# Kernel tuning notes

Hardware: AMD Instinct MI355X
Metric: run time of the kernel (lower is better)

Reference implementation:

```python
import jax, jax.numpy as jnp
import numpy as np

B, S, H, F, E, TOP_K = 2, 2048, 1024, 2048, 8, 2


def setup_inputs() -> dict:
    key = jax.random.key(0)
    ks = jax.random.split(key, 5)
    scale_h = 1.0 / np.sqrt(H)
    scale_f = 1.0 / np.sqrt(F)
    return {
        "hidden_states": jax.random.normal(ks[0], (B, S, H), jnp.float32),
        "gate_w": jax.random.normal(ks[1], (H, E), jnp.float32) * scale_h,
        "w_up": jax.random.normal(ks[2], (E, H, F), jnp.float32) * scale_h,
        "w_gate": jax.random.normal(ks[3], (E, H, F), jnp.float32) * scale_h,
        "w_down": jax.random.normal(ks[4], (E, F, H), jnp.float32) * scale_f,
    }


def reference(hidden_states, gate_w, w_up, w_gate, w_down):
    b, s, h = hidden_states.shape
    x = hidden_states.reshape(-1, h)                      # [T, H]
    T = x.shape[0]

    # Router: softmax then top-k then renormalize (as in the module)
    router_logits = x @ gate_w                            # [T, E]
    probs = jax.nn.softmax(router_logits, axis=-1)
    routing_weights, selected_experts = jax.lax.top_k(probs, TOP_K)  # [T, K]
    routing_weights = routing_weights / jnp.sum(routing_weights, axis=-1, keepdims=True)
    routing_weights = routing_weights.astype(x.dtype)

    # Per-token combine weight for each expert (sum over k where selected == e).
    # Equals the masked where/+ accumulation in the original (zero where unselected).
    combine = jnp.zeros((T, E), x.dtype).at[
        jnp.arange(T)[:, None], selected_experts
    ].add(routing_weights)                                # [T, E]

    # Dense expert compute on ALL tokens for every expert (faithful to original,
    # where each device runs its expert on the full token set, then psum).
    up = jnp.einsum("th,ehf->etf", x, w_up)               # [E, T, F]
    gate = jnp.einsum("th,ehf->etf", x, w_gate)           # [E, T, F]
    inner = jax.nn.silu(up) * gate                        # note: silu on up_proj, as in source
    expert_out = jnp.einsum("etf,efh->eth", inner, w_down)  # [E, T, H]

    # Weighted combine == psum over expert axis of masked/weighted outputs.
    y = jnp.einsum("te,eth->th", combine, expert_out)     # [T, H]
    return y.reshape(b, s, h)
```

## Files before the change

### kernel.cpp

```cpp
#include <hip/hip_runtime.h>
#include <hip/hip_bf16.h>

typedef __bf16 bf16x8 __attribute__((ext_vector_type(8)));
typedef float f32x4 __attribute__((ext_vector_type(4)));

#define T_TOK 4096
#define H_DIM 1024
#define F_DIM 2048
#define NEXP 8
#define TOTROWS 8192
#define MAXTILES 80

__device__ inline unsigned short f2b(float f) {
    unsigned int u = __float_as_uint(f);
    unsigned int r = (u + 0x7fffu + ((u >> 16) & 1u)) >> 16;
    return (unsigned short)r;
}

__device__ inline void gload16(const void* g, void* l) {
    __builtin_amdgcn_global_load_lds(
        (const __attribute__((address_space(1))) unsigned int*)g,
        (__attribute__((address_space(3))) unsigned int*)l,
        16, 0, 0);
}

__global__ __launch_bounds__(256) void router_kernel(const float* __restrict__ x,
                                                     const float* __restrict__ gw,
                                                     int* __restrict__ sel, float* __restrict__ selw) {
    int t = blockIdx.x * 4 + (threadIdx.x >> 6);
    int lane = threadIdx.x & 63;
    float acc[8] = {0.f,0.f,0.f,0.f,0.f,0.f,0.f,0.f};
    const float* xr = x + (size_t)t * H_DIM;
    for (int h = lane; h < H_DIM; h += 64) {
        float xv = xr[h];
        const float4* g = (const float4*)(gw + h * 8);
        float4 g0 = g[0], g1 = g[1];
        acc[0] += xv * g0.x; acc[1] += xv * g0.y; acc[2] += xv * g0.z; acc[3] += xv * g0.w;
        acc[4] += xv * g1.x; acc[5] += xv * g1.y; acc[6] += xv * g1.z; acc[7] += xv * g1.w;
    }
#pragma unroll
    for (int off = 32; off >= 1; off >>= 1)
#pragma unroll
        for (int e = 0; e < 8; ++e)
            acc[e] += __shfl_down(acc[e], off);
    if (lane == 0) {
        float mx = acc[0];
#pragma unroll
        for (int e = 1; e < 8; ++e) mx = fmaxf(mx, acc[e]);
        float p[8]; float s = 0.f;
#pragma unroll
        for (int e = 0; e < 8; ++e) { p[e] = expf(acc[e] - mx); s += p[e]; }
        float inv_s = 1.f / s;
#pragma unroll
        for (int e = 0; e < 8; ++e) p[e] *= inv_s;
        int e1 = 0; float p1 = p[0];
#pragma unroll
        for (int e = 1; e < 8; ++e) if (p[e] > p1) { p1 = p[e]; e1 = e; }
        int e2 = -1; float p2 = -1.f;
#pragma unroll
        for (int e = 0; e < 8; ++e) { if (e == e1) continue; if (p[e] > p2) { p2 = p[e]; e2 = e; } }
        float inv = 1.f / (p1 + p2);
        sel[t * 2 + 0] = e1; sel[t * 2 + 1] = e2;
        selw[t * 2 + 0] = p1 * inv; selw[t * 2 + 1] = p2 * inv;
    }
}

__global__ __launch_bounds__(256) void scan_kernel(const int* __restrict__ sel,
                                                   int* __restrict__ cnt, int* __restrict__ off,
                                                   int* __restrict__ fill,
                                                   int* __restrict__ tileExp, int* __restrict__ tileM0) {
    __shared__ int h[NEXP];
    int tid = threadIdx.x;
    if (tid < NEXP) h[tid] = 0;
    __syncthreads();
    for (int i = tid; i < TOTROWS; i += 256) atomicAdd(&h[sel[i]], 1);
    __syncthreads();
    if (tid == 0) {
        int o = 0;
        for (int e = 0; e < NEXP; ++e) { cnt[e] = h[e]; off[e] = o; o += h[e]; fill[e] = 0; }
        int nt = 0;
        for (int e = 0; e < NEXP; ++e)
            for (int m0 = 0; m0 < h[e]; m0 += 128) { tileExp[nt] = e; tileM0[nt] = m0; nt++; }
        for (int i = nt; i < MAXTILES; ++i) { tileExp[i] = -1; tileM0[i] = 0; }
    }
}

__global__ __launch_bounds__(256) void scatgath_kernel(const int* __restrict__ sel,
                                                       const float* __restrict__ selw,
                                                       const int* __restrict__ off,
                                                       int* __restrict__ fill,
                                                       float* __restrict__ rowWgt,
                                                       int* __restrict__ tokRow,
                                                       const float* __restrict__ x,
                                                       unsigned short* __restrict__ Xg) {
    __shared__ int rs[2];
    int t = blockIdx.x;
    int tid = threadIdx.x;
    if (tid == 0) {
#pragma unroll
        for (int k = 0; k < 2; ++k) {
            int e = sel[t * 2 + k];
            int slot = atomicAdd(&fill[e], 1);
            int r = off[e] + slot;
            rowWgt[r] = selw[t * 2 + k];
            tokRow[t * 2 + k] = r;
            rs[k] = r;
        }
    }
    __syncthreads();
    int r1 = rs[0], r2 = rs[1];
    float4 v = ((const float4*)(x + (size_t)t * H_DIM))[tid];
    ushort4 o;
    o.x = f2b(v.x); o.y = f2b(v.y); o.z = f2b(v.z); o.w = f2b(v.w);
    ((ushort4*)(Xg + (size_t)r1 * H_DIM))[tid] = o;
    ((ushort4*)(Xg + (size_t)r2 * H_DIM))[tid] = o;
}

__global__ __launch_bounds__(256) void transpose_cvt_kernel(
        const float* __restrict__ w_up, const float* __restrict__ w_gate,
        const float* __restrict__ w_down,
        unsigned short* __restrict__ wTu, unsigned short* __restrict__ wTg,
        unsigned short* __restrict__ wTd) {
    __shared__ unsigned short lt[64 * 68];
    int z = blockIdx.z;
    int e = blockIdx.y;
    const float* src; unsigned short* dst; int R, C, tr, tc;
    if (z == 0)      { src = w_up;   dst = wTu; R = H_DIM; C = F_DIM; }
    else if (z == 1) { src = w_gate; dst = wTg; R = H_DIM; C = F_DIM; }
    else             { src = w_down; dst = wTd; R = F_DIM; C = H_DIM; }
    if (R == H_DIM) { tc = blockIdx.x & 31; tr = blockIdx.x >> 5; }
    else            { tc = blockIdx.x & 15; tr = blockIdx.x >> 4; }
    const float* s = src + (size_t)e * H_DIM * F_DIM;
    unsigned short* d = dst + (size_t)e * H_DIM * F_DIM;
    int r0 = tr * 64, c0 = tc * 64;
    int tid = threadIdx.x;
    int fc = tid & 15, row = tid >> 4;
#pragma unroll
    for (int i = 0; i < 4; ++i) {
        int r = row + i * 16;
        float4 v = *(const float4*)(s + (size_t)(r0 + r) * C + c0 + fc * 4);
        lt[(fc * 4 + 0) * 68 + r] = f2b(v.x);
        lt[(fc * 4 + 1) * 68 + r] = f2b(v.y);
        lt[(fc * 4 + 2) * 68 + r] = f2b(v.z);
        lt[(fc * 4 + 3) * 68 + r] = f2b(v.w);
    }
    __syncthreads();
    int ch = tid & 7, cc = tid >> 3;
#pragma unroll
    for (int i = 0; i < 2; ++i) {
        int c = cc + i * 32;
        uint2 lo = *(const uint2*)&lt[c * 68 + ch * 8];
        uint2 hi = *(const uint2*)&lt[c * 68 + ch * 8 + 4];
        uint4 o = make_uint4(lo.x, lo.y, hi.x, hi.y);
        *(uint4*)(d + (size_t)(c0 + c) * R + r0 + ch * 8) = o;
    }
}

__global__ __launch_bounds__(256, 2) void gemm_upgate_kernel(
        const unsigned short* __restrict__ Xg,
        const unsigned short* __restrict__ wTu,
        const unsigned short* __restrict__ wTg,
        unsigned short* __restrict__ inner,
        const int* __restrict__ tileExp, const int* __restrict__ tileM0,
        const int* __restrict__ off, const int* __restrict__ cnt) {
    __shared__ __align__(16) unsigned short la[128 * 64];
    __shared__ __align__(16) unsigned short lbu[128 * 64];
    __shared__ __align__(16) unsigned short lbg[128 * 64];
    int bt = blockIdx.y;
    int e = tileExp[bt];
    if (e < 0) return;
    int m0 = tileM0[bt];
    int r0 = off[e] + m0;
    int valid = cnt[e] - m0;
    int f0 = blockIdx.x * 128;
    const unsigned short* aB = Xg + (size_t)r0 * H_DIM;
    const unsigned short* bu = wTu + (size_t)e * F_DIM * H_DIM + (size_t)f0 * H_DIM;
    const unsigned short* bg = wTg + (size_t)e * F_DIM * H_DIM + (size_t)f0 * H_DIM;
    int tid = threadIdx.x;
    int lane = tid & 63, wid = tid >> 6;
    int wm = wid >> 1, wn = wid & 1;
    int l16 = lane & 15, quad = lane >> 4;

    int srcOff[4];
#pragma unroll
    for (int it = 0; it < 4; ++it) {
        int chunk = it * 256 + tid;
        int row = chunk >> 3;
        srcOff[it] = row * H_DIM + (((chunk & 7) ^ (row & 7)) << 3);
    }
    f32x4 accU[4][4], accG[4][4];
#pragma unroll
    for (int i = 0; i < 4; ++i)
#pragma unroll
        for (int j = 0; j < 4; ++j) { accU[i][j] = (f32x4)0.f; accG[i][j] = (f32x4)0.f; }

    for (int k0 = 0; k0 < H_DIM; k0 += 64) {
        __syncthreads();
#pragma unroll
        for (int it = 0; it < 4; ++it) {
            int lbase = it * 2048 + wid * 512;
            gload16(aB + srcOff[it] + k0, &la[lbase]);
            gload16(bu + srcOff[it] + k0, &lbu[lbase]);
            gload16(bg + srcOff[it] + k0, &lbg[lbase]);
        }
        __syncthreads();
#pragma unroll
        for (int h = 0; h < 2; ++h) {
            bf16x8 af[4], bfu[4], bfg[4];
#pragma unroll
            for (int i = 0; i < 4; ++i) {
                int lr = wm * 64 + i * 16 + l16;
                af[i] = *(const bf16x8*)&la[lr * 64 + ((((h * 4 + quad) ^ (lr & 7))) << 3)];
            }
#pragma unroll
            for (int j = 0; j < 4; ++j) {
                int lr = wn * 64 + j * 16 + l16;
                int p = lr * 64 + ((((h * 4 + quad) ^ (lr & 7))) << 3);
                bfu[j] = *(const bf16x8*)&lbu[p];
                bfg[j] = *(const bf16x8*)&lbg[p];
            }
#pragma unroll
            for (int i = 0; i < 4; ++i)
#pragma unroll
                for (int j = 0; j < 4; ++j) {
                    accU[i][j] = __builtin_amdgcn_mfma_f32_16x16x32_bf16(af[i], bfu[j], accU[i][j], 0, 0, 0);
                    accG[i][j] = __builtin_amdgcn_mfma_f32_16x16x32_bf16(af[i], bfg[j], accG[i][j], 0, 0, 0);
                }
        }
    }
#pragma unroll
    for (int i = 0; i < 4; ++i) {
#pragma unroll
        for (int rr = 0; rr < 4; ++rr) {
            int ml = wm * 64 + i * 16 + quad * 4 + rr;
            if (ml >= valid) continue;
            size_t base = (size_t)(r0 + ml) * F_DIM + f0;
#pragma unroll
            for (int j = 0; j < 4; ++j) {
                float u = accU[i][j][rr];
                float g = accG[i][j][rr];
                float v = u / (1.f + expf(-u)) * g;
                inner[base + wn * 64 + j * 16 + l16] = f2b(v);
            }
        }
    }
}

__global__ __launch_bounds__(256, 2) void gemm_down_kernel(
        const unsigned short* __restrict__ inner,
        const unsigned short* __restrict__ wTd,
        float* __restrict__ part,
        const int* __restrict__ tileExp, const int* __restrict__ tileM0,
        const int* __restrict__ off, const int* __restrict__ cnt,
        const float* __restrict__ rowWgt) {
    __shared__ __align__(16) unsigned short la[128 * 64];
    __shared__ __align__(16) unsigned short lb[128 * 64];
    int bt = blockIdx.y;
    int e = tileExp[bt];
    if (e < 0) return;
    int m0 = tileM0[bt];
    int r0 = off[e] + m0;
    int valid = cnt[e] - m0;
    int h0 = blockIdx.x * 128;
    const unsigned short* aB = inner + (size_t)r0 * F_DIM;
    const unsigned short* bp = wTd + (size_t)e * H_DIM * F_DIM + (size_t)h0 * F_DIM;
    int tid = threadIdx.x;
    int lane = tid & 63, wid = tid >> 6;
    int wm = wid >> 1, wn = wid & 1;
    int l16 = lane & 15, quad = lane >> 4;

    int srcOff[4];
#pragma unroll
    for (int it = 0; it < 4; ++it) {
        int chunk = it * 256 + tid;
        int row = chunk >> 3;
        srcOff[it] = row * F_DIM + (((chunk & 7) ^ (row & 7)) << 3);
    }
    f32x4 acc[4][4];
#pragma unroll
    for (int i = 0; i < 4; ++i)
#pragma unroll
        for (int j = 0; j < 4; ++j) acc[i][j] = (f32x4)0.f;

    for (int k0 = 0; k0 < F_DIM; k0 += 64) {
        __syncthreads();
#pragma unroll
        for (int it = 0; it < 4; ++it) {
            int lbase = it * 2048 + wid * 512;
            gload16(aB + srcOff[it] + k0, &la[lbase]);
            gload16(bp + srcOff[it] + k0, &lb[lbase]);
        }
        __syncthreads();
#pragma unroll
        for (int h = 0; h < 2; ++h) {
            bf16x8 af[4], bf[4];
#pragma unroll
            for (int i = 0; i < 4; ++i) {
                int lr = wm * 64 + i * 16 + l16;
                af[i] = *(const bf16x8*)&la[lr * 64 + ((((h * 4 + quad) ^ (lr & 7))) << 3)];
            }
#pragma unroll
            for (int j = 0; j < 4; ++j) {
                int lr = wn * 64 + j * 16 + l16;
                bf[j] = *(const bf16x8*)&lb[lr * 64 + ((((h * 4 + quad) ^ (lr & 7))) << 3)];
            }
#pragma unroll
            for (int i = 0; i < 4; ++i)
#pragma unroll
                for (int j = 0; j < 4; ++j)
                    acc[i][j] = __builtin_amdgcn_mfma_f32_16x16x32_bf16(af[i], bf[j], acc[i][j], 0, 0, 0);
        }
    }
#pragma unroll
    for (int i = 0; i < 4; ++i) {
#pragma unroll
        for (int rr = 0; rr < 4; ++rr) {
            int ml = wm * 64 + i * 16 + quad * 4 + rr;
            if (ml >= valid) continue;
            int gr = r0 + ml;
            float w = rowWgt[gr];
            float* orow = part + (size_t)gr * H_DIM + h0;
#pragma unroll
            for (int j = 0; j < 4; ++j)
                orow[wn * 64 + j * 16 + l16] = w * acc[i][j][rr];
        }
    }
}

__global__ __launch_bounds__(256) void combine_kernel(const float* __restrict__ part,
                                                      const int* __restrict__ tokRow,
                                                      float* __restrict__ out) {
    int t = blockIdx.x;
    int r1 = tokRow[t * 2 + 0], r2 = tokRow[t * 2 + 1];
    int i = threadIdx.x;
    float4 a = ((const float4*)(part + (size_t)r1 * H_DIM))[i];
    float4 b = ((const float4*)(part + (size_t)r2 * H_DIM))[i];
    float4 o;
    o.x = a.x + b.x; o.y = a.y + b.y; o.z = a.z + b.z; o.w = a.w + b.w;
    ((float4*)(out + (size_t)t * H_DIM))[i] = o;
}

extern "C" void kernel_launch(void* const* d_in, const int* in_sizes, int n_in,
                              void* d_out, int out_size, void* d_ws, size_t ws_size,
                              hipStream_t stream) {
    const float* x      = (const float*)d_in[0];
    const float* gw     = (const float*)d_in[1];
    const float* w_up   = (const float*)d_in[2];
    const float* w_gate = (const float*)d_in[3];
    const float* w_down = (const float*)d_in[4];
    float* out = (float*)d_out;

    char* ws = (char*)d_ws;
    size_t o = 0;
    unsigned short* wTu = (unsigned short*)(ws + o); o += (size_t)NEXP * F_DIM * H_DIM * 2;
    unsigned short* wTg = (unsigned short*)(ws + o); o += (size_t)NEXP * F_DIM * H_DIM * 2;
    unsigned short* wTd = (unsigned short*)(ws + o); o += (size_t)NEXP * H_DIM * F_DIM * 2;
    unsigned short* Xg  = (unsigned short*)(ws + o); o += (size_t)TOTROWS * H_DIM * 2;
    unsigned short* inner = (unsigned short*)(ws + o); o += (size_t)TOTROWS * F_DIM * 2;
    o += 1024 * 1024;
    float* rowWgt = (float*)(ws + o); o += TOTROWS * 4;
    int*   tokRow = (int*)(ws + o);   o += T_TOK * 2 * 4;
    int*   sel    = (int*)(ws + o);   o += T_TOK * 2 * 4;
    float* selw   = (float*)(ws + o); o += T_TOK * 2 * 4;
    int*   cnt    = (int*)(ws + o);   o += 8 * 4;
    int*   fill   = (int*)(ws + o);   o += 8 * 4;
    int*   off_   = (int*)(ws + o);   o += 8 * 4;
    int*   tileExp = (int*)(ws + o);  o += MAXTILES * 4;
    int*   tileM0  = (int*)(ws + o);  o += MAXTILES * 4;
    float* part = (float*)wTu;

    router_kernel<<<T_TOK / 4, 256, 0, stream>>>(x, gw, sel, selw);
    scan_kernel<<<1, 256, 0, stream>>>(sel, cnt, off_, fill, tileExp, tileM0);
    scatgath_kernel<<<T_TOK, 256, 0, stream>>>(sel, selw, off_, fill, rowWgt, tokRow, x, Xg);
    transpose_cvt_kernel<<<dim3(512, NEXP, 3), 256, 0, stream>>>(w_up, w_gate, w_down, wTu, wTg, wTd);
    gemm_upgate_kernel<<<dim3(F_DIM / 128, 72), 256, 0, stream>>>(Xg, wTu, wTg, inner, tileExp, tileM0, off_, cnt);
    gemm_down_kernel<<<dim3(H_DIM / 128, 72), 256, 0, stream>>>(inner, wTd, part, tileExp, tileM0, off_, cnt, rowWgt);
    combine_kernel<<<T_TOK, 256, 0, stream>>>(part, tokRow, out);
}
```

Before: 507.7 us.

## Double-buffer LDS tiles in expert GEMMs with k-major layout

Both expert GEMM kernels now use two LDS buffers, so the global-to-LDS loads for the next k-slice are issued before computing on the current one. This overlaps memory latency with MFMA work and cuts one barrier per iteration. The LDS layout changes from a row-major XOR swizzle to a k-chunk-major layout (chunk*1024 + row*8). The up/gate kernel also halves its k-step to 32 to keep shared memory at 48KB, and its SiLU now uses fast exp and a hardware reciprocal. The down kernel's LDS grows to 64KB per block, which may limit residency to two blocks per CU.

```diff
diff --git a/kernel.cpp b/kernel.cpp
--- a/kernel.cpp
+++ b/kernel.cpp
@@ -163,9 +163,9 @@
         unsigned short* __restrict__ inner,
         const int* __restrict__ tileExp, const int* __restrict__ tileM0,
         const int* __restrict__ off, const int* __restrict__ cnt) {
-    __shared__ __align__(16) unsigned short la[128 * 64];
-    __shared__ __align__(16) unsigned short lbu[128 * 64];
-    __shared__ __align__(16) unsigned short lbg[128 * 64];
+    __shared__ __align__(16) unsigned short la[2][4096];
+    __shared__ __align__(16) unsigned short lbu[2][4096];
+    __shared__ __align__(16) unsigned short lbg[2][4096];
     int bt = blockIdx.y;
     int e = tileExp[bt];
     if (e < 0) return;
@@ -181,12 +181,12 @@
     int wm = wid >> 1, wn = wid & 1;
     int l16 = lane & 15, quad = lane >> 4;
 
-    int srcOff[4];
-#pragma unroll
-    for (int it = 0; it < 4; ++it) {
-        int chunk = it * 256 + tid;
-        int row = chunk >> 3;
-        srcOff[it] = row * H_DIM + (((chunk & 7) ^ (row & 7)) << 3);
+    int sOff[2], lb_[2];
+#pragma unroll
+    for (int it = 0; it < 2; ++it) {
+        int p = it * 256 + tid;
+        sOff[it] = (p & 127) * H_DIM + ((p >> 7) << 3);
+        lb_[it] = it * 2048 + wid * 512;
     }
     f32x4 accU[4][4], accG[4][4];
 #pragma unroll
@@ -194,39 +194,45 @@
 #pragma unroll
         for (int j = 0; j < 4; ++j) { accU[i][j] = (f32x4)0.f; accG[i][j] = (f32x4)0.f; }
 
-    for (int k0 = 0; k0 < H_DIM; k0 += 64) {
+    int aRd = quad * 1024 + (wm * 64 + l16) * 8;
+    int bRd = quad * 1024 + (wn * 64 + l16) * 8;
+
+#pragma unroll
+    for (int it = 0; it < 2; ++it) {
+        gload16(aB + sOff[it], &la[0][lb_[it]]);
+        gload16(bu + sOff[it], &lbu[0][lb_[it]]);
+        gload16(bg + sOff[it], &lbg[0][lb_[it]]);
+    }
+    __syncthreads();
+
+    int cur = 0;
+    for (int k0 = 32; k0 <= H_DIM; k0 += 32) {
+        int nxt = cur ^ 1;
+        if (k0 < H_DIM) {
+#pragma unroll
+            for (int it = 0; it < 2; ++it) {
+                gload16(aB + sOff[it] + k0, &la[nxt][lb_[it]]);
+                gload16(bu + sOff[it] + k0, &lbu[nxt][lb_[it]]);
+                gload16(bg + sOff[it] + k0, &lbg[nxt][lb_[it]]);
+            }
+        }
+        bf16x8 af[4], bfu[4], bfg[4];
+#pragma unroll
+        for (int i = 0; i < 4; ++i) af[i] = *(const bf16x8*)&la[cur][aRd + i * 128];
+#pragma unroll
+        for (int j = 0; j < 4; ++j) {
+            bfu[j] = *(const bf16x8*)&lbu[cur][bRd + j * 128];
+            bfg[j] = *(const bf16x8*)&lbg[cur][bRd + j * 128];
+        }
+#pragma unroll
+        for (int i = 0; i < 4; ++i)
+#pragma unroll
+            for (int j = 0; j < 4; ++j) {
+                accU[i][j] = __builtin_amdgcn_mfma_f32_16x16x32_bf16(af[i], bfu[j], accU[i][j], 0, 0, 0);
+                accG[i][j] = __builtin_amdgcn_mfma_f32_16x16x32_bf16(af[i], bfg[j], accG[i][j], 0, 0, 0);
+            }
         __syncthreads();
-#pragma unroll
-        for (int it = 0; it < 4; ++it) {
-            int lbase = it * 2048 + wid * 512;
-            gload16(aB + srcOff[it] + k0, &la[lbase]);
-            gload16(bu + srcOff[it] + k0, &lbu[lbase]);
-            gload16(bg + srcOff[it] + k0, &lbg[lbase]);
-        }
-        __syncthreads();
-#pragma unroll
-        for (int h = 0; h < 2; ++h) {
-            bf16x8 af[4], bfu[4], bfg[4];
-#pragma unroll
-            for (int i = 0; i < 4; ++i) {
-                int lr = wm * 64 + i * 16 + l16;
-                af[i] = *(const bf16x8*)&la[lr * 64 + ((((h * 4 + quad) ^ (lr & 7))) << 3)];
-            }
-#pragma unroll
-            for (int j = 0; j < 4; ++j) {
-                int lr = wn * 64 + j * 16 + l16;
-                int p = lr * 64 + ((((h * 4 + quad) ^ (lr & 7))) << 3);
-                bfu[j] = *(const bf16x8*)&lbu[p];
-                bfg[j] = *(const bf16x8*)&lbg[p];
-            }
-#pragma unroll
-            for (int i = 0; i < 4; ++i)
-#pragma unroll
-                for (int j = 0; j < 4; ++j) {
-                    accU[i][j] = __builtin_amdgcn_mfma_f32_16x16x32_bf16(af[i], bfu[j], accU[i][j], 0, 0, 0);
-                    accG[i][j] = __builtin_amdgcn_mfma_f32_16x16x32_bf16(af[i], bfg[j], accG[i][j], 0, 0, 0);
-                }
-        }
+        cur = nxt;
     }
 #pragma unroll
     for (int i = 0; i < 4; ++i) {
@@ -239,7 +245,7 @@
             for (int j = 0; j < 4; ++j) {
                 float u = accU[i][j][rr];
                 float g = accG[i][j][rr];
-                float v = u / (1.f + expf(-u)) * g;
+                float v = u * __builtin_amdgcn_rcpf(1.f + __expf(-u)) * g;
                 inner[base + wn * 64 + j * 16 + l16] = f2b(v);
             }
         }
@@ -253,8 +259,8 @@
         const int* __restrict__ tileExp, const int* __restrict__ tileM0,
         const int* __restrict__ off, const int* __restrict__ cnt,
         const float* __restrict__ rowWgt) {
-    __shared__ __align__(16) unsigned short la[128 * 64];
-    __shared__ __align__(16) unsigned short lb[128 * 64];
+    __shared__ __align__(16) unsigned short la[2][8192];
+    __shared__ __align__(16) unsigned short lb[2][8192];
     int bt = blockIdx.y;
     int e = tileExp[bt];
     if (e < 0) return;
@@ -269,12 +275,12 @@
     int wm = wid >> 1, wn = wid & 1;
     int l16 = lane & 15, quad = lane >> 4;
 
-    int srcOff[4];
+    int sOff[4], lb_[4];
 #pragma unroll
     for (int it = 0; it < 4; ++it) {
-        int chunk = it * 256 + tid;
-        int row = chunk >> 3;
-        srcOff[it] = row * F_DIM + (((chunk & 7) ^ (row & 7)) << 3);
+        int p = it * 256 + tid;
+        sOff[it] = (p & 127) * F_DIM + ((p >> 7) << 3);
+        lb_[it] = it * 2048 + wid * 512;
     }
     f32x4 acc[4][4];
 #pragma unroll
@@ -282,34 +288,43 @@
 #pragma unroll
         for (int j = 0; j < 4; ++j) acc[i][j] = (f32x4)0.f;
 
-    for (int k0 = 0; k0 < F_DIM; k0 += 64) {
-        __syncthreads();
-#pragma unroll
-        for (int it = 0; it < 4; ++it) {
-            int lbase = it * 2048 + wid * 512;
-            gload16(aB + srcOff[it] + k0, &la[lbase]);
-            gload16(bp + srcOff[it] + k0, &lb[lbase]);
-        }
-        __syncthreads();
+    int aRd = (wm * 64 + l16) * 8;
+    int bRd = (wn * 64 + l16) * 8;
+
+#pragma unroll
+    for (int it = 0; it < 4; ++it) {
+        gload16(aB + sOff[it], &la[0][lb_[it]]);
+        gload16(bp + sOff[it], &lb[0][lb_[it]]);
+    }
+    __syncthreads();
+
+    int cur = 0;
+    for (int k0 = 64; k0 <= F_DIM; k0 += 64) {
+        int nxt = cur ^ 1;
+        if (k0 < F_DIM) {
+#pragma unroll
+            for (int it = 0; it < 4; ++it) {
+                gload16(aB + sOff[it] + k0, &la[nxt][lb_[it]]);
+                gload16(bp + sOff[it] + k0, &lb[nxt][lb_[it]]);
+            }
+        }
 #pragma unroll
         for (int h = 0; h < 2; ++h) {
             bf16x8 af[4], bf[4];
 #pragma unroll
-            for (int i = 0; i < 4; ++i) {
-                int lr = wm * 64 + i * 16 + l16;
-                af[i] = *(const bf16x8*)&la[lr * 64 + ((((h * 4 + quad) ^ (lr & 7))) << 3)];
-            }
-#pragma unroll
-            for (int j = 0; j < 4; ++j) {
-                int lr = wn * 64 + j * 16 + l16;
-                bf[j] = *(const bf16x8*)&lb[lr * 64 + ((((h * 4 + quad) ^ (lr & 7))) << 3)];
-            }
+            for (int i = 0; i < 4; ++i)
+                af[i] = *(const bf16x8*)&la[cur][(h * 4 + quad) * 1024 + aRd + i * 128];
+#pragma unroll
+            for (int j = 0; j < 4; ++j)
+                bf[j] = *(const bf16x8*)&lb[cur][(h * 4 + quad) * 1024 + bRd + j * 128];
 #pragma unroll
             for (int i = 0; i < 4; ++i)
 #pragma unroll
                 for (int j = 0; j < 4; ++j)
                     acc[i][j] = __builtin_amdgcn_mfma_f32_16x16x32_bf16(af[i], bf[j], acc[i][j], 0, 0, 0);
         }
+        __syncthreads();
+        cur = nxt;
     }
 #pragma unroll
     for (int i = 0; i < 4; ++i) {
```

Measured after the change: 641.2 us. 1.26x slower.

## Multi-buffer LDS in expert GEMMs with async global-to-LDS prefetch pipelining

Applied to the files above, without the earlier changes.

Rewrites the K loops of the up/gate and down expert GEMMs as software pipelines. The up/gate kernel gets a 3-stage LDS ring and the down kernel a 2-stage ring, with explicit vmcnt waits and raw s_barrier calls, so global-to-LDS loads for later K tiles overlap MFMA compute on the current tile. The up/gate kernel's LDS use triples, so its launch bounds drop to one block per CU, trading occupancy for in-block latency hiding. SiLU also switches to fast exp and a reciprocal intrinsic, at some cost in precision.

```diff
diff --git a/kernel.cpp b/kernel.cpp
--- a/kernel.cpp
+++ b/kernel.cpp
@@ -156,16 +156,65 @@
     }
 }
 
-__global__ __launch_bounds__(256, 2) void gemm_upgate_kernel(
+#define UPG_STAGE(K0, B) do {                                               \
+    _Pragma("unroll")                                                       \
+    for (int it_ = 0; it_ < 4; ++it_) {                                     \
+        gload16(aB + sOff[it_] + (K0), &la[B][lb_[it_]]);                   \
+        gload16(buW + sOff[it_] + (K0), &lbu[B][lb_[it_]]);                 \
+        gload16(bgW + sOff[it_] + (K0), &lbg[B][lb_[it_]]);                 \
+    }                                                                       \
+} while (0)
+
+#define UPG_COMPUTE(B) do {                                                 \
+    _Pragma("unroll")                                                       \
+    for (int h_ = 0; h_ < 2; ++h_) {                                        \
+        bf16x8 af_[4], bu_[4], bg_[4];                                      \
+        _Pragma("unroll")                                                   \
+        for (int i_ = 0; i_ < 4; ++i_) {                                    \
+            int lr = wm * 64 + i_ * 16 + l16;                               \
+            af_[i_] = *(const bf16x8*)&la[B][lr * 64 + (((h_ * 4 + quad) ^ (lr & 7)) << 3)]; \
+        }                                                                   \
+        _Pragma("unroll")                                                   \
+        for (int j_ = 0; j_ < 4; ++j_) {                                    \
+            int lr = wn * 64 + j_ * 16 + l16;                               \
+            int p_ = lr * 64 + (((h_ * 4 + quad) ^ (lr & 7)) << 3);         \
+            bu_[j_] = *(const bf16x8*)&lbu[B][p_];                          \
+            bg_[j_] = *(const bf16x8*)&lbg[B][p_];                          \
+        }                                                                   \
+        _Pragma("unroll")                                                   \
+        for (int i_ = 0; i_ < 4; ++i_)                                      \
+            _Pragma("unroll")                                               \
+            for (int j_ = 0; j_ < 4; ++j_) {                                \
+                accU[i_][j_] = __builtin_amdgcn_mfma_f32_16x16x32_bf16(af_[i_], bu_[j_], accU[i_][j_], 0, 0, 0); \
+                accG[i_][j_] = __builtin_amdgcn_mfma_f32_16x16x32_bf16(af_[i_], bg_[j_], accG[i_][j_], 0, 0, 0); \
+            }                                                               \
+    }                                                                       \
+} while (0)
+
+#define UPG_STEP(T, B) do {                                                 \
+    int t_ = (T);                                                           \
+    if (t_ <= 13)      asm volatile("s_waitcnt vmcnt(24)" ::: "memory");    \
+    else if (t_ == 14) asm volatile("s_waitcnt vmcnt(12)" ::: "memory");    \
+    else               asm volatile("s_waitcnt vmcnt(0)"  ::: "memory");    \
+    __builtin_amdgcn_s_barrier();                                           \
+    __builtin_amdgcn_sched_barrier(0);                                      \
+    UPG_COMPUTE(B);                                                         \
+    __builtin_amdgcn_sched_barrier(0);                                      \
+    __builtin_amdgcn_s_barrier();                                           \
+    __builtin_amdgcn_sched_barrier(0);                                      \
+    if (t_ + 3 < 16) UPG_STAGE((t_ + 3) * 64, B);                           \
+} while (0)
+
+__global__ __launch_bounds__(256, 1) void gemm_upgate_kernel(
         const unsigned short* __restrict__ Xg,
         const unsigned short* __restrict__ wTu,
         const unsigned short* __restrict__ wTg,
         unsigned short* __restrict__ inner,
         const int* __restrict__ tileExp, const int* __restrict__ tileM0,
         const int* __restrict__ off, const int* __restrict__ cnt) {
-    __shared__ __align__(16) unsigned short la[128 * 64];
-    __shared__ __align__(16) unsigned short lbu[128 * 64];
-    __shared__ __align__(16) unsigned short lbg[128 * 64];
+    __shared__ __align__(16) unsigned short la[3][8192];
+    __shared__ __align__(16) unsigned short lbu[3][8192];
+    __shared__ __align__(16) unsigned short lbg[3][8192];
     int bt = blockIdx.y;
     int e = tileExp[bt];
     if (e < 0) return;
@@ -173,20 +222,21 @@
     int r0 = off[e] + m0;
     int valid = cnt[e] - m0;
     int f0 = blockIdx.x * 128;
-    const unsigned short* aB = Xg + (size_t)r0 * H_DIM;
-    const unsigned short* bu = wTu + (size_t)e * F_DIM * H_DIM + (size_t)f0 * H_DIM;
-    const unsigned short* bg = wTg + (size_t)e * F_DIM * H_DIM + (size_t)f0 * H_DIM;
+    const unsigned short* aB  = Xg + (size_t)r0 * H_DIM;
+    const unsigned short* buW = wTu + (size_t)e * F_DIM * H_DIM + (size_t)f0 * H_DIM;
+    const unsigned short* bgW = wTg + (size_t)e * F_DIM * H_DIM + (size_t)f0 * H_DIM;
     int tid = threadIdx.x;
     int lane = tid & 63, wid = tid >> 6;
     int wm = wid >> 1, wn = wid & 1;
     int l16 = lane & 15, quad = lane >> 4;
 
-    int srcOff[4];
+    int sOff[4], lb_[4];
 #pragma unroll
     for (int it = 0; it < 4; ++it) {
         int chunk = it * 256 + tid;
         int row = chunk >> 3;
-        srcOff[it] = row * H_DIM + (((chunk & 7) ^ (row & 7)) << 3);
+        sOff[it] = row * H_DIM + (((chunk & 7) ^ (row & 7)) << 3);
+        lb_[it] = it * 2048 + wid * 512;
     }
     f32x4 accU[4][4], accG[4][4];
 #pragma unroll
@@ -194,40 +244,17 @@
 #pragma unroll
         for (int j = 0; j < 4; ++j) { accU[i][j] = (f32x4)0.f; accG[i][j] = (f32x4)0.f; }
 
-    for (int k0 = 0; k0 < H_DIM; k0 += 64) {
-        __syncthreads();
-#pragma unroll
-        for (int it = 0; it < 4; ++it) {
-            int lbase = it * 2048 + wid * 512;
-            gload16(aB + srcOff[it] + k0, &la[lbase]);
-            gload16(bu + srcOff[it] + k0, &lbu[lbase]);
-            gload16(bg + srcOff[it] + k0, &lbg[lbase]);
-        }
-        __syncthreads();
-#pragma unroll
-        for (int h = 0; h < 2; ++h) {
-            bf16x8 af[4], bfu[4], bfg[4];
-#pragma unroll
-            for (int i = 0; i < 4; ++i) {
-                int lr = wm * 64 + i * 16 + l16;
-                af[i] = *(const bf16x8*)&la[lr * 64 + ((((h * 4 + quad) ^ (lr & 7))) << 3)];
-            }
-#pragma unroll
-            for (int j = 0; j < 4; ++j) {
-                int lr = wn * 64 + j * 16 + l16;
-                int p = lr * 64 + ((((h * 4 + quad) ^ (lr & 7))) << 3);
-                bfu[j] = *(const bf16x8*)&lbu[p];
-                bfg[j] = *(const bf16x8*)&lbg[p];
-            }
-#pragma unroll
-            for (int i = 0; i < 4; ++i)
-#pragma unroll
-                for (int j = 0; j < 4; ++j) {
-                    accU[i][j] = __builtin_amdgcn_mfma_f32_16x16x32_bf16(af[i], bfu[j], accU[i][j], 0, 0, 0);
-                    accG[i][j] = __builtin_amdgcn_mfma_f32_16x16x32_bf16(af[i], bfg[j], accG[i][j], 0, 0, 0);
-                }
-        }
-    }
+    UPG_STAGE(0, 0);
+    UPG_STAGE(64, 1);
+    UPG_STAGE(128, 2);
+
+    for (int t = 0; t < 15; t += 3) {
+        UPG_STEP(t,     0);
+        UPG_STEP(t + 1, 1);
+        UPG_STEP(t + 2, 2);
+    }
+    UPG_STEP(15, 0);
+
 #pragma unroll
     for (int i = 0; i < 4; ++i) {
 #pragma unroll
@@ -239,12 +266,55 @@
             for (int j = 0; j < 4; ++j) {
                 float u = accU[i][j][rr];
                 float g = accG[i][j][rr];
-                float v = u / (1.f + expf(-u)) * g;
+                float v = u * __builtin_amdgcn_rcpf(1.f + __expf(-u)) * g;
                 inner[base + wn * 64 + j * 16 + l16] = f2b(v);
             }
         }
     }
 }
+
+#define DWN_STAGE(K0, B) do {                                               \
+    _Pragma("unroll")                                                       \
+    for (int it_ = 0; it_ < 4; ++it_) {                                     \
+        gload16(aB + sOff[it_] + (K0), &la[B][lb_[it_]]);                   \
+        gload16(bp + sOff[it_] + (K0), &lb[B][lb_[it_]]);                   \
+    }                                                                       \
+} while (0)
+
+#define DWN_COMPUTE(B) do {                                                 \
+    _Pragma("unroll")                                                       \
+    for (int h_ = 0; h_ < 2; ++h_) {                                        \
+        bf16x8 af_[4], bw_[4];                                              \
+        _Pragma("unroll")                                                   \
+        for (int i_ = 0; i_ < 4; ++i_) {                                    \
+            int lr = wm * 64 + i_ * 16 + l16;                               \
+            af_[i_] = *(const bf16x8*)&la[B][lr * 64 + (((h_ * 4 + quad) ^ (lr & 7)) << 3)]; \
+        }                                                                   \
+        _Pragma("unroll")                                                   \
+        for (int j_ = 0; j_ < 4; ++j_) {                                    \
+            int lr = wn * 64 + j_ * 16 + l16;                               \
+            bw_[j_] = *(const bf16x8*)&lb[B][lr * 64 + (((h_ * 4 + quad) ^ (lr & 7)) << 3)]; \
+        }                                                                   \
+        _Pragma("unroll")                                                   \
+        for (int i_ = 0; i_ < 4; ++i_)                                      \
+            _Pragma("unroll")                                               \
+            for (int j_ = 0; j_ < 4; ++j_)                                  \
+                acc[i_][j_] = __builtin_amdgcn_mfma_f32_16x16x32_bf16(af_[i_], bw_[j_], acc[i_][j_], 0, 0, 0); \
+    }                                                                       \
+} while (0)
+
+#define DWN_STEP(T, B) do {                                                 \
+    int t_ = (T);                                                           \
+    if (t_ != 31) asm volatile("s_waitcnt vmcnt(8)" ::: "memory");          \
+    else          asm volatile("s_waitcnt vmcnt(0)" ::: "memory");          \
+    __builtin_amdgcn_s_barrier();                                           \
+    __builtin_amdgcn_sched_barrier(0);                                      \
+    DWN_COMPUTE(B);                                                         \
+    __builtin_amdgcn_sched_barrier(0);                                      \
+    __builtin_amdgcn_s_barrier();                                           \
+    __builtin_amdgcn_sched_barrier(0);                                      \
+    if (t_ + 2 < 32) DWN_STAGE((t_ + 2) * 64, B);                           \
+} while (0)
 
 __global__ __launch_bounds__(256, 2) void gemm_down_kernel(
         const unsigned short* __restrict__ inner,
@@ -253,8 +323,8 @@
         const int* __restrict__ tileExp, const int* __restrict__ tileM0,
         const int* __restrict__ off, const int* __restrict__ cnt,
         const float* __restrict__ rowWgt) {
-    __shared__ __align__(16) unsigned short la[128 * 64];
-    __shared__ __align__(16) unsigned short lb[128 * 64];
+    __shared__ __align__(16) unsigned short la[2][8192];
+    __shared__ __align__(16) unsigned short lb[2][8192];
     int bt = blockIdx.y;
     int e = tileExp[bt];
     if (e < 0) return;
@@ -269,12 +339,13 @@
     int wm = wid >> 1, wn = wid & 1;
     int l16 = lane & 15, quad = lane >> 4;
 
-    int srcOff[4];
+    int sOff[4], lb_[4];
 #pragma unroll
     for (int it = 0; it < 4; ++it) {
         int chunk = it * 256 + tid;
         int row = chunk >> 3;
-        srcOff[it] = row * F_DIM + (((chunk & 7) ^ (row & 7)) << 3);
+        sOff[it] = row * F_DIM + (((chunk & 7) ^ (row & 7)) << 3);
+        lb_[it] = it * 2048 + wid * 512;
     }
     f32x4 acc[4][4];
 #pragma unroll
@@ -282,35 +353,14 @@
 #pragma unroll
         for (int j = 0; j < 4; ++j) acc[i][j] = (f32x4)0.f;
 
-    for (int k0 = 0; k0 < F_DIM; k0 += 64) {
-        __syncthreads();
-#pragma unroll
-        for (int it = 0; it < 4; ++it) {
-            int lbase = it * 2048 + wid * 512;
-            gload16(aB + srcOff[it] + k0, &la[lbase]);
-            gload16(bp + srcOff[it] + k0, &lb[lbase]);
-        }
-        __syncthreads();
-#pragma unroll
-        for (int h = 0; h < 2; ++h) {
-            bf16x8 af[4], bf[4];
-#pragma unroll
-            for (int i = 0; i < 4; ++i) {
-                int lr = wm * 64 + i * 16 + l16;
-                af[i] = *(const bf16x8*)&la[lr * 64 + ((((h * 4 + quad) ^ (lr & 7))) << 3)];
-            }
-#pragma unroll
-            for (int j = 0; j < 4; ++j) {
-                int lr = wn * 64 + j * 16 + l16;
-                bf[j] = *(const bf16x8*)&lb[lr * 64 + ((((h * 4 + quad) ^ (lr & 7))) << 3)];
-            }
-#pragma unroll
-            for (int i = 0; i < 4; ++i)
-#pragma unroll
-                for (int j = 0; j < 4; ++j)
-                    acc[i][j] = __builtin_amdgcn_mfma_f32_16x16x32_bf16(af[i], bf[j], acc[i][j], 0, 0, 0);
-        }
-    }
+    DWN_STAGE(0, 0);
+    DWN_STAGE(64, 1);
+
+    for (int t = 0; t < 32; t += 2) {
+        DWN_STEP(t,     0);
+        DWN_STEP(t + 1, 1);
+    }
+
 #pragma unroll
     for (int i = 0; i < 4; ++i) {
 #pragma unroll
```

After: 574.8 us. 13.2% more time.

## Double-buffer both expert GEMMs with async LDS prefetch and larger up/gate tiles

Applied to the files above, without the earlier changes.

Both expert GEMMs now use two LDS buffers. The next K-slice is issued through global_load_lds while MFMAs run on the current one, paced by explicit vmcnt waits, barriers and setprio. The up/gate kernel moves to 512 threads with 256-row M tiles, which halves the weight re-reads per token, and the scan kernel builds a separate 256-row tile list for it. The down kernel uses 512 threads over a 4x2 wave grid, and SiLU switches to fast exp/rcp intrinsics. The trade-off is more LDS per block, which can lower occupancy, and padding waste on partial 256-row tiles.

```diff
diff --git a/kernel.cpp b/kernel.cpp
--- a/kernel.cpp
+++ b/kernel.cpp
@@ -10,6 +10,7 @@
 #define NEXP 8
 #define TOTROWS 8192
 #define MAXTILES 80
+#define UPT 40
 
 __device__ inline unsigned short f2b(float f) {
     unsigned int u = __float_as_uint(f);
@@ -68,7 +69,8 @@
 __global__ __launch_bounds__(256) void scan_kernel(const int* __restrict__ sel,
                                                    int* __restrict__ cnt, int* __restrict__ off,
                                                    int* __restrict__ fill,
-                                                   int* __restrict__ tileExp, int* __restrict__ tileM0) {
+                                                   int* __restrict__ tileExp, int* __restrict__ tileM0,
+                                                   int* __restrict__ tileExpU, int* __restrict__ tileM0U) {
     __shared__ int h[NEXP];
     int tid = threadIdx.x;
     if (tid < NEXP) h[tid] = 0;
@@ -82,6 +84,10 @@
         for (int e = 0; e < NEXP; ++e)
             for (int m0 = 0; m0 < h[e]; m0 += 128) { tileExp[nt] = e; tileM0[nt] = m0; nt++; }
         for (int i = nt; i < MAXTILES; ++i) { tileExp[i] = -1; tileM0[i] = 0; }
+        int nu = 0;
+        for (int e = 0; e < NEXP; ++e)
+            for (int m0 = 0; m0 < h[e]; m0 += 256) { tileExpU[nu] = e; tileM0U[nu] = m0; nu++; }
+        for (int i = nu; i < UPT; ++i) { tileExpU[i] = -1; tileM0U[i] = 0; }
     }
 }
 
@@ -156,37 +162,82 @@
     }
 }
 
-__global__ __launch_bounds__(256, 2) void gemm_upgate_kernel(
+#define UPG_STAGE(K0, B) do {                                                \
+    _Pragma("unroll")                                                        \
+    for (int it_ = 0; it_ < 4; ++it_)                                        \
+        gload16(aB + sOffA[it_] + (K0), &la[B][lbA[it_]]);                   \
+    _Pragma("unroll")                                                        \
+    for (int it_ = 0; it_ < 2; ++it_) {                                      \
+        gload16(buW + sOffB[it_] + (K0), &lbu[B][lbB[it_]]);                 \
+        gload16(bgW + sOffB[it_] + (K0), &lbg[B][lbB[it_]]);                 \
+    }                                                                        \
+} while (0)
+
+#define UPG_COMPUTE(B) do {                                                  \
+    _Pragma("unroll")                                                        \
+    for (int h_ = 0; h_ < 2; ++h_) {                                         \
+        bf16x8 af_[4], bu_[4], bg_[4];                                       \
+        _Pragma("unroll")                                                    \
+        for (int i_ = 0; i_ < 4; ++i_) {                                     \
+            int lr = wm * 64 + i_ * 16 + l16;                                \
+            af_[i_] = *(const bf16x8*)&la[B][lr * 64 + (((h_ * 4 + quad) ^ (lr & 7)) << 3)]; \
+        }                                                                    \
+        _Pragma("unroll")                                                    \
+        for (int j_ = 0; j_ < 4; ++j_) {                                     \
+            int lr = wn * 64 + j_ * 16 + l16;                                \
+            int p_ = lr * 64 + (((h_ * 4 + quad) ^ (lr & 7)) << 3);          \
+            bu_[j_] = *(const bf16x8*)&lbu[B][p_];                           \
+            bg_[j_] = *(const bf16x8*)&lbg[B][p_];                           \
+        }                                                                    \
+        _Pragma("unroll")                                                    \
+        for (int i_ = 0; i_ < 4; ++i_)                                       \
+            _Pragma("unroll")                                                \
+            for (int j_ = 0; j_ < 4; ++j_) {                                 \
+                accU[i_][j_] = __builtin_amdgcn_mfma_f32_16x16x32_bf16(af_[i_], bu_[j_], accU[i_][j_], 0, 0, 0); \
+                accG[i_][j_] = __builtin_amdgcn_mfma_f32_16x16x32_bf16(af_[i_], bg_[j_], accG[i_][j_], 0, 0, 0); \
+            }                                                                \
+    }                                                                        \
+} while (0)
+
+__global__ __launch_bounds__(512, 2) void gemm_upgate_kernel(
         const unsigned short* __restrict__ Xg,
         const unsigned short* __restrict__ wTu,
         const unsigned short* __restrict__ wTg,
         unsigned short* __restrict__ inner,
-        const int* __restrict__ tileExp, const int* __restrict__ tileM0,
+        const int* __restrict__ tileExpU, const int* __restrict__ tileM0U,
         const int* __restrict__ off, const int* __restrict__ cnt) {
-    __shared__ __align__(16) unsigned short la[128 * 64];
-    __shared__ __align__(16) unsigned short lbu[128 * 64];
-    __shared__ __align__(16) unsigned short lbg[128 * 64];
+    __shared__ __align__(16) unsigned short la[2][16384];
+    __shared__ __align__(16) unsigned short lbu[2][8192];
+    __shared__ __align__(16) unsigned short lbg[2][8192];
     int bt = blockIdx.y;
-    int e = tileExp[bt];
+    int e = tileExpU[bt];
     if (e < 0) return;
-    int m0 = tileM0[bt];
+    int m0 = tileM0U[bt];
     int r0 = off[e] + m0;
     int valid = cnt[e] - m0;
     int f0 = blockIdx.x * 128;
-    const unsigned short* aB = Xg + (size_t)r0 * H_DIM;
-    const unsigned short* bu = wTu + (size_t)e * F_DIM * H_DIM + (size_t)f0 * H_DIM;
-    const unsigned short* bg = wTg + (size_t)e * F_DIM * H_DIM + (size_t)f0 * H_DIM;
+    const unsigned short* aB  = Xg + (size_t)r0 * H_DIM;
+    const unsigned short* buW = wTu + (size_t)e * F_DIM * H_DIM + (size_t)f0 * H_DIM;
+    const unsigned short* bgW = wTg + (size_t)e * F_DIM * H_DIM + (size_t)f0 * H_DIM;
     int tid = threadIdx.x;
     int lane = tid & 63, wid = tid >> 6;
     int wm = wid >> 1, wn = wid & 1;
     int l16 = lane & 15, quad = lane >> 4;
 
-    int srcOff[4];
+    int sOffA[4], lbA[4], sOffB[2], lbB[2];
 #pragma unroll
     for (int it = 0; it < 4; ++it) {
-        int chunk = it * 256 + tid;
+        int chunk = it * 512 + tid;
         int row = chunk >> 3;
-        srcOff[it] = row * H_DIM + (((chunk & 7) ^ (row & 7)) << 3);
+        sOffA[it] = row * H_DIM + (((chunk & 7) ^ (row & 7)) << 3);
+        lbA[it] = it * 4096 + wid * 512;
+    }
+#pragma unroll
+    for (int it = 0; it < 2; ++it) {
+        int chunk = it * 512 + tid;
+        int row = chunk >> 3;
+        sOffB[it] = row * H_DIM + (((chunk & 7) ^ (row & 7)) << 3);
+        lbB[it] = it * 4096 + wid * 512;
     }
     f32x4 accU[4][4], accG[4][4];
 #pragma unroll
@@ -194,40 +245,31 @@
 #pragma unroll
         for (int j = 0; j < 4; ++j) { accU[i][j] = (f32x4)0.f; accG[i][j] = (f32x4)0.f; }
 
-    for (int k0 = 0; k0 < H_DIM; k0 += 64) {
-        __syncthreads();
-#pragma unroll
-        for (int it = 0; it < 4; ++it) {
-            int lbase = it * 2048 + wid * 512;
-            gload16(aB + srcOff[it] + k0, &la[lbase]);
-            gload16(bu + srcOff[it] + k0, &lbu[lbase]);
-            gload16(bg + srcOff[it] + k0, &lbg[lbase]);
-        }
-        __syncthreads();
-#pragma unroll
-        for (int h = 0; h < 2; ++h) {
-            bf16x8 af[4], bfu[4], bfg[4];
-#pragma unroll
-            for (int i = 0; i < 4; ++i) {
-                int lr = wm * 64 + i * 16 + l16;
-                af[i] = *(const bf16x8*)&la[lr * 64 + ((((h * 4 + quad) ^ (lr & 7))) << 3)];
-            }
-#pragma unroll
-            for (int j = 0; j < 4; ++j) {
-                int lr = wn * 64 + j * 16 + l16;
-                int p = lr * 64 + ((((h * 4 + quad) ^ (lr & 7))) << 3);
-                bfu[j] = *(const bf16x8*)&lbu[p];
-                bfg[j] = *(const bf16x8*)&lbg[p];
-            }
-#pragma unroll
-            for (int i = 0; i < 4; ++i)
-#pragma unroll
-                for (int j = 0; j < 4; ++j) {
-                    accU[i][j] = __builtin_amdgcn_mfma_f32_16x16x32_bf16(af[i], bfu[j], accU[i][j], 0, 0, 0);
-                    accG[i][j] = __builtin_amdgcn_mfma_f32_16x16x32_bf16(af[i], bfg[j], accG[i][j], 0, 0, 0);
-                }
-        }
-    }
+    UPG_STAGE(0, 0);
+    UPG_STAGE(64, 1);
+
+    for (int t = 0; t < 14; ++t) {
+        asm volatile("s_waitcnt vmcnt(8)" ::: "memory");
+        __builtin_amdgcn_s_barrier();
+        __builtin_amdgcn_sched_barrier(0);
+        __builtin_amdgcn_s_setprio(1);
+        UPG_COMPUTE(t & 1);
+        __builtin_amdgcn_s_setprio(0);
+        __builtin_amdgcn_sched_barrier(0);
+        __builtin_amdgcn_s_barrier();
+        __builtin_amdgcn_sched_barrier(0);
+        UPG_STAGE((t + 2) * 64, t & 1);
+    }
+    asm volatile("s_waitcnt vmcnt(8)" ::: "memory");
+    __builtin_amdgcn_s_barrier();
+    __builtin_amdgcn_sched_barrier(0);
+    UPG_COMPUTE(0);
+    __builtin_amdgcn_s_barrier();
+    asm volatile("s_waitcnt vmcnt(0)" ::: "memory");
+    __builtin_amdgcn_s_barrier();
+    __builtin_amdgcn_sched_barrier(0);
+    UPG_COMPUTE(1);
+
 #pragma unroll
     for (int i = 0; i < 4; ++i) {
 #pragma unroll
@@ -239,22 +281,52 @@
             for (int j = 0; j < 4; ++j) {
                 float u = accU[i][j][rr];
                 float g = accG[i][j][rr];
-                float v = u / (1.f + expf(-u)) * g;
+                float v = u * __builtin_amdgcn_rcpf(1.f + __expf(-u)) * g;
                 inner[base + wn * 64 + j * 16 + l16] = f2b(v);
             }
         }
     }
 }
 
-__global__ __launch_bounds__(256, 2) void gemm_down_kernel(
+#define DWN_STAGE(K0, B) do {                                                \
+    _Pragma("unroll")                                                        \
+    for (int it_ = 0; it_ < 2; ++it_) {                                      \
+        gload16(aB + sOff[it_] + (K0), &la[B][lb_[it_]]);                    \
+        gload16(bp + sOff[it_] + (K0), &lb[B][lb_[it_]]);                    \
+    }                                                                        \
+} while (0)
+
+#define DWN_COMPUTE(B) do {                                                  \
+    _Pragma("unroll")                                                        \
+    for (int h_ = 0; h_ < 2; ++h_) {                                         \
+        bf16x8 af_[4], bw_[2];                                               \
+        _Pragma("unroll")                                                    \
+        for (int i_ = 0; i_ < 4; ++i_) {                                     \
+            int lr = wm * 64 + i_ * 16 + l16;                                \
+            af_[i_] = *(const bf16x8*)&la[B][lr * 64 + (((h_ * 4 + quad) ^ (lr & 7)) << 3)]; \
+        }                                                                    \
+        _Pragma("unroll")                                                    \
+        for (int j_ = 0; j_ < 2; ++j_) {                                     \
+            int lr = wn * 32 + j_ * 16 + l16;                                \
+            bw_[j_] = *(const bf16x8*)&lb[B][lr * 64 + (((h_ * 4 + quad) ^ (lr & 7)) << 3)]; \
+        }                                                                    \
+        _Pragma("unroll")                                                    \
+        for (int i_ = 0; i_ < 4; ++i_)                                       \
+            _Pragma("unroll")                                                \
+            for (int j_ = 0; j_ < 2; ++j_)                                   \
+                acc[i_][j_] = __builtin_amdgcn_mfma_f32_16x16x32_bf16(af_[i_], bw_[j_], acc[i_][j_], 0, 0, 0); \
+    }                                                                        \
+} while (0)
+
+__global__ __launch_bounds__(512, 4) void gemm_down_kernel(
         const unsigned short* __restrict__ inner,
         const unsigned short* __restrict__ wTd,
         float* __restrict__ part,
         const int* __restrict__ tileExp, const int* __restrict__ tileM0,
         const int* __restrict__ off, const int* __restrict__ cnt,
         const float* __restrict__ rowWgt) {
-    __shared__ __align__(16) unsigned short la[128 * 64];
-    __shared__ __align__(16) unsigned short lb[128 * 64];
+    __shared__ __align__(16) unsigned short la[2][8192];
+    __shared__ __align__(16) unsigned short lb[2][8192];
     int bt = blockIdx.y;
     int e = tileExp[bt];
     if (e < 0) return;
@@ -266,51 +338,48 @@
     const unsigned short* bp = wTd + (size_t)e * H_DIM * F_DIM + (size_t)h0 * F_DIM;
     int tid = threadIdx.x;
     int lane = tid & 63, wid = tid >> 6;
-    int wm = wid >> 1, wn = wid & 1;
+    int wm = wid >> 2, wn = wid & 3;
     int l16 = lane & 15, quad = lane >> 4;
 
-    int srcOff[4];
-#pragma unroll
-    for (int it = 0; it < 4; ++it) {
-        int chunk = it * 256 + tid;
+    int sOff[2], lb_[2];
+#pragma unroll
+    for (int it = 0; it < 2; ++it) {
+        int chunk = it * 512 + tid;
         int row = chunk >> 3;
-        srcOff[it] = row * F_DIM + (((chunk & 7) ^ (row & 7)) << 3);
-    }
-    f32x4 acc[4][4];
+        sOff[it] = row * F_DIM + (((chunk & 7) ^ (row & 7)) << 3);
+        lb_[it] = it * 4096 + wid * 512;
+    }
+    f32x4 acc[4][2];
 #pragma unroll
     for (int i = 0; i < 4; ++i)
 #pragma unroll
-        for (int j = 0; j < 4; ++j) acc[i][j] = (f32x4)0.f;
-
-    for (int k0 = 0; k0 < F_DIM; k0 += 64) {
-        __syncthreads();
-#pragma unroll
-        for (int it = 0; it < 4; ++it) {
-            int lbase = it * 2048 + wid * 512;
-            gload16(aB + srcOff[it] + k0, &la[lbase]);
-            gload16(bp + srcOff[it] + k0, &lb[lbase]);
-        }
-        __syncthreads();
-#pragma unroll
-        for (int h = 0; h < 2; ++h) {
-            bf16x8 af[4], bf[4];
-#pragma unroll
-            for (int i = 0; i < 4; ++i) {
-                int lr = wm * 64 + i * 16 + l16;
-                af[i] = *(const bf16x8*)&la[lr * 64 + ((((h * 4 + quad) ^ (lr & 7))) << 3)];
-            }
-#pragma unroll
-            for (int j = 0; j < 4; ++j) {
-                int lr = wn * 64 + j * 16 + l16;
-                bf[j] = *(const bf16x8*)&lb[lr * 64 + ((((h * 4 + quad) ^ (lr & 7))) << 3)];
-            }
-#pragma unroll
-            for (int i = 0; i < 4; ++i)
-#pragma unroll
-                for (int j = 0; j < 4; ++j)
-                    acc[i][j] = __builtin_amdgcn_mfma_f32_16x16x32_bf16(af[i], bf[j], acc[i][j], 0, 0, 0);
-        }
-    }
+        for (int j = 0; j < 2; ++j) acc[i][j] = (f32x4)0.f;
+
+    DWN_STAGE(0, 0);
+    DWN_STAGE(64, 1);
+
+    for (int t = 0; t < 30; ++t) {
+        asm volatile("s_waitcnt vmcnt(4)" ::: "memory");
+        __builtin_amdgcn_s_barrier();
+        __builtin_amdgcn_sched_barrier(0);
+        __builtin_amdgcn_s_setprio(1);
+        DWN_COMPUTE(t & 1);
+        __builtin_amdgcn_s_setprio(0);
+        __builtin_amdgcn_sched_barrier(0);
+        __builtin_amdgcn_s_barrier();
+        __builtin_amdgcn_sched_barrier(0);
+        DWN_STAGE((t + 2) * 64, t & 1);
+    }
+    asm volatile("s_waitcnt vmcnt(4)" ::: "memory");
+    __builtin_amdgcn_s_barrier();
+    __builtin_amdgcn_sched_barrier(0);
+    DWN_COMPUTE(0);
+    __builtin_amdgcn_s_barrier();
+    asm volatile("s_waitcnt vmcnt(0)" ::: "memory");
+    __builtin_amdgcn_s_barrier();
+    __builtin_amdgcn_sched_barrier(0);
+    DWN_COMPUTE(1);
+
 #pragma unroll
     for (int i = 0; i < 4; ++i) {
 #pragma unroll
@@ -321,8 +390,8 @@
             float w = rowWgt[gr];
             float* orow = part + (size_t)gr * H_DIM + h0;
 #pragma unroll
-            for (int j = 0; j < 4; ++j)
-                orow[wn * 64 + j * 16 + l16] = w * acc[i][j][rr];
+            for (int j = 0; j < 2; ++j)
+                orow[wn * 32 + j * 16 + l16] = w * acc[i][j][rr];
         }
     }
 }
@@ -357,7 +426,7 @@
     unsigned short* wTd = (unsigned short*)(ws + o); o += (size_t)NEXP * H_DIM * F_DIM * 2;
     unsigned short* Xg  = (unsigned short*)(ws + o); o += (size_t)TOTROWS * H_DIM * 2;
     unsigned short* inner = (unsigned short*)(ws + o); o += (size_t)TOTROWS * F_DIM * 2;
-    o += 1024 * 1024;
+    o += 2 * 1024 * 1024;
     float* rowWgt = (float*)(ws + o); o += TOTROWS * 4;
     int*   tokRow = (int*)(ws + o);   o += T_TOK * 2 * 4;
     int*   sel    = (int*)(ws + o);   o += T_TOK * 2 * 4;
@@ -367,13 +436,15 @@
     int*   off_   = (int*)(ws + o);   o += 8 * 4;
     int*   tileExp = (int*)(ws + o);  o += MAXTILES * 4;
     int*   tileM0  = (int*)(ws + o);  o += MAXTILES * 4;
+    int*   tileExpU = (int*)(ws + o); o += UPT * 4;
+    int*   tileM0U  = (int*)(ws + o); o += UPT * 4;
     float* part = (float*)wTu;
 
     router_kernel<<<T_TOK / 4, 256, 0, stream>>>(x, gw, sel, selw);
-    scan_kernel<<<1, 256, 0, stream>>>(sel, cnt, off_, fill, tileExp, tileM0);
+    scan_kernel<<<1, 256, 0, stream>>>(sel, cnt, off_, fill, tileExp, tileM0, tileExpU, tileM0U);
     scatgath_kernel<<<T_TOK, 256, 0, stream>>>(sel, selw, off_, fill, rowWgt, tokRow, x, Xg);
     transpose_cvt_kernel<<<dim3(512, NEXP, 3), 256, 0, stream>>>(w_up, w_gate, w_down, wTu, wTg, wTd);
-    gemm_upgate_kernel<<<dim3(F_DIM / 128, 72), 256, 0, stream>>>(Xg, wTu, wTg, inner, tileExp, tileM0, off_, cnt);
-    gemm_down_kernel<<<dim3(H_DIM / 128, 72), 256, 0, stream>>>(inner, wTd, part, tileExp, tileM0, off_, cnt, rowWgt);
+    gemm_upgate_kernel<<<dim3(F_DIM / 128, UPT), 512, 0, stream>>>(Xg, wTu, wTg, inner, tileExpU, tileM0U, off_, cnt);
+    gemm_down_kernel<<<dim3(H_DIM / 128, 72), 512, 0, stream>>>(inner, wTd, part, tileExp, tileM0, off_, cnt, rowWgt);
     combine_kernel<<<T_TOK, 256, 0, stream>>>(part, tokRow, out);
 }
```

Result: slower. 532.5 us (+4.9%).
